# Performance work log

Hardware: AMD Instinct MI355X
Metric: run time of the kernel (lower is better)

Reference implementation:

```python
import jax, jax.numpy as jnp
import numpy as np

N, P, E = 100000, 10000, 500000
DN, DP, DK, SKIP, MLP_H = 256, 128, 100, 27, 64
E_MEAN, E_STD = 4.0, 2.0
ETA_MEAN, ETA_STD = 0.0, 1.5
ATT_NORM = 0.1  # 1/sqrt(100)
LN_EPS, RMS_EPS = 1e-5, 1e-6


def setup_inputs() -> dict:
    key = jax.random.key(0)
    ks = jax.random.split(key, 32)
    DIN = DN + SKIP  # 283
    s = 0.05
    inp = {
        'node_hidden': jax.random.normal(ks[0], (N, DN), jnp.float32),
        'energy': jax.random.uniform(ks[1], (N,), jnp.float32, 0.01, 1.0),
        'eta': jax.random.normal(ks[2], (N,), jnp.float32),
        'phi': jax.random.normal(ks[3], (N,), jnp.float32),
        'layer': jax.random.uniform(ks[4], (N,), jnp.float32),
        'eta_l': jax.random.normal(ks[5], (N, 6), jnp.float32),
        'phi_l': jax.random.normal(ks[6], (N, 6), jnp.float32),
        'ene_l': jax.random.normal(ks[7], (N, 6), jnp.float32),
        'track_feats': jax.random.uniform(ks[8], (N, 5), jnp.float32),
        'particle_hidden': jax.random.normal(ks[9], (P, DP), jnp.float32),
        'global_rep': jax.random.normal(ks[10], (P, DN), jnp.float32),
        'edge_src': jax.random.randint(ks[11], (E,), 0, N, jnp.int32),
        'edge_dst': jax.random.randint(ks[12], (E,), 0, P, jnp.int32),
        # learned params
        'W_key': jax.random.normal(ks[13], (DIN, DK), jnp.float32) * s,
        'b_key': jnp.zeros((DK,), jnp.float32),
        'W_val': jax.random.normal(ks[14], (DIN, DP), jnp.float32) * s,
        'b_val': jnp.zeros((DP,), jnp.float32),
        'W_q': jax.random.normal(ks[15], (DP + DN, DK), jnp.float32) * s,
        'b_q': jnp.zeros((DK,), jnp.float32),
        'W_ih': jax.random.normal(ks[16], (DP, 3 * DP), jnp.float32) * s,
        'b_ih': jnp.zeros((3 * DP,), jnp.float32),
        'W_hh': jax.random.normal(ks[17], (DP, 3 * DP), jnp.float32) * s,
        'b_hh': jnp.zeros((3 * DP,), jnp.float32),
        'ln_g': jnp.ones((DP,), jnp.float32),
        'ln_b': jnp.zeros((DP,), jnp.float32),
        'W1': jax.random.normal(ks[18], (DP, MLP_H), jnp.float32) * s,
        'b1': jnp.zeros((MLP_H,), jnp.float32),
        'W2': jax.random.normal(ks[19], (MLP_H, DP), jnp.float32) * s,
        'b2': jnp.zeros((DP,), jnp.float32),
        'rms_w': jnp.ones((DP,), jnp.float32),
        'lin_w': jax.random.normal(ks[20], (1, DP), jnp.float32),
    }
    return inp


def _forward(node_hidden, energy, eta, phi, layer, eta_l, phi_l, ene_l, track_feats,
             particle_hidden, global_rep,
             W_key, b_key, W_val, b_val, W_q, b_q, W_ih, b_ih, W_hh, b_hh,
             ln_g, ln_b, W1, b1, W2, b2, rms_w, lin_w, edge_src, edge_dst):
    # --- build node inputs: hidden rep + 27 skip scalars (same order as torch cat) ---
    skip = jnp.concatenate([
        ((jnp.log(energy) - E_MEAN) / E_STD)[:, None],
        ((eta - ETA_MEAN) / ETA_STD)[:, None],
        phi[:, None], layer[:, None],
        (eta_l - ETA_MEAN) / ETA_STD,  # eta_l1..l6
        phi_l, ene_l,
        track_feats,  # isTrack, nTracks, tracks_pt, nTracks_4, tracks_pt_4
    ], axis=1)  # [N, 27]
    x = jnp.concatenate([node_hidden, skip], axis=1)  # [N, 283]
    keys = x @ W_key + b_key      # [N, 100]
    vals = x @ W_val + b_val      # [N, DP]
    q = jnp.concatenate([particle_hidden, global_rep], axis=1) @ W_q + b_q  # [P, 100]

    # --- per-edge attention (note: node_update consumes RAW relu attention) ---
    att = jax.nn.relu(jnp.sum(keys[edge_src] * q[edge_dst], axis=1) * ATT_NORM)  # [E]
    msg = att[:, None] * vals[edge_src]                                          # [E, DP]
    ws = jax.ops.segment_sum(msg, edge_dst, num_segments=P)                      # [P, DP]

    # --- node update: rmsnorm * sigmoid(eltwise) gating, GRU, LN, MLP residual ---
    rms = ws * jax.lax.rsqrt(jnp.mean(ws * ws, axis=-1, keepdims=True) + RMS_EPS) * rms_w
    gated = rms * jax.nn.sigmoid(ws * lin_w)

    h = particle_hidden
    gi = gated @ W_ih + b_ih
    gh = h @ W_hh + b_hh
    i_r, i_z, i_n = jnp.split(gi, 3, axis=1)
    h_r, h_z, h_n = jnp.split(gh, 3, axis=1)
    r = jax.nn.sigmoid(i_r + h_r)
    z = jax.nn.sigmoid(i_z + h_z)
    n = jnp.tanh(i_n + r * h_n)
    h_new = (1.0 - z) * n + z * h

    mu = jnp.mean(h_new, axis=-1, keepdims=True)
    var = jnp.mean((h_new - mu) ** 2, axis=-1, keepdims=True)
    ln = (h_new - mu) * jax.lax.rsqrt(var + LN_EPS) * ln_g + ln_b
    mlp = jax.nn.relu(ln @ W1 + b1) @ W2 + b2
    return h + mlp  # updated particle 'node hidden rep'


def reference(node_hidden, energy, eta, phi, layer, eta_l, phi_l, ene_l, track_feats,
              particle_hidden, global_rep, edge_src, edge_dst,
              W_key, b_key, W_val, b_val, W_q, b_q, W_ih, b_ih, W_hh, b_hh,
              ln_g, ln_b, W1, b1, W2, b2, rms_w, lin_w):
    return _forward(node_hidden, energy, eta, phi, layer, eta_l, phi_l, ene_l, track_feats,
                    particle_hidden, global_rep,
                    W_key, b_key, W_val, b_val, W_q, b_q, W_ih, b_ih, W_hh, b_hh,
                    ln_g, ln_b, W1, b1, W2, b2, rms_w, lin_w, edge_src, edge_dst)
```

## Files before the change

kernel.cpp:

```cpp
#include <hip/hip_runtime.h>
#include <hip/hip_bf16.h>
#include <math.h>

#define THREADS 256

typedef __bf16 bf16_t;
typedef __bf16 bf16x8 __attribute__((ext_vector_type(8)));
typedef float f32x4 __attribute__((ext_vector_type(4)));

__device__ __forceinline__ float sigmoidf_(float x) { return 1.f / (1.f + expf(-x)); }

__device__ __forceinline__ void gload_lds16(const void* g, void* l) {
    __builtin_amdgcn_global_load_lds((const __attribute__((address_space(1))) void*)g,
                                     (__attribute__((address_space(3))) void*)l, 16, 0, 0);
}

__device__ __forceinline__ bf16x8 cvt8(float4 a, float4 b) {
    bf16x8 v;
    v[0] = (bf16_t)a.x; v[1] = (bf16_t)a.y; v[2] = (bf16_t)a.z; v[3] = (bf16_t)a.w;
    v[4] = (bf16_t)b.x; v[5] = (bf16_t)b.y; v[6] = (bf16_t)b.z; v[7] = (bf16_t)b.w;
    return v;
}

__global__ void prep_kernel(const float* __restrict__ W_key, const float* __restrict__ W_val,
                            const float* __restrict__ W_q, const float* __restrict__ b_key,
                            const float* __restrict__ b_val, const float* __restrict__ b_q,
                            bf16_t* __restrict__ WbfT, bf16_t* __restrict__ WqT,
                            float* __restrict__ bpn, float* __restrict__ bpq)
{
    int i = blockIdx.x * THREADS + threadIdx.x;
    const int NW = 256 * 288, NQ = 128 * 384;
    if (i < NW) {
        int c = i / 288, k = i - c * 288;
        float v = 0.f;
        if (k < 283) {
            if (c < 100) v = W_key[k * 100 + c];
            else if (c >= 128 && c < 256) v = W_val[k * 128 + (c - 128)];
        }
        WbfT[i] = (bf16_t)v;
    } else if (i < NW + NQ) {
        int j = i - NW;
        int c = j / 384, k = j - c * 384;
        WqT[j] = (bf16_t)((c < 100) ? W_q[k * 100 + c] : 0.f);
    } else if (i < NW + NQ + 256) {
        int c = i - NW - NQ;
        bpn[c] = (c < 100) ? b_key[c] : ((c >= 128 && c < 256) ? b_val[c - 128] : 0.f);
    } else if (i < NW + NQ + 256 + 128) {
        int c = i - NW - NQ - 256;
        bpq[c] = (c < 100) ? b_q[c] : 0.f;
    }
}

__global__ void prep2_kernel(const float* __restrict__ W_ih, const float* __restrict__ W_hh,
                             const float* __restrict__ b_ih, const float* __restrict__ b_hh,
                             const float* __restrict__ W1, const float* __restrict__ b1,
                             const float* __restrict__ W2,
                             bf16_t* __restrict__ BTg, bf16_t* __restrict__ W1Tp,
                             bf16_t* __restrict__ W2Tp, float* __restrict__ bgru,
                             float* __restrict__ b1p)
{
    int i = blockIdx.x * THREADS + threadIdx.x;
    const int NG = 768 * 256, N1 = 128 * 128, N2 = 128 * 128;
    if (i < NG) {
        int c = i >> 8, k = i & 255;
        float v = 0.f;
        if (c < 384) { if (k < 128) v = W_ih[k * 384 + c]; }
        else         { if (k >= 128) v = W_hh[(k - 128) * 384 + (c - 384)]; }
        BTg[i] = (bf16_t)v;
    } else if (i < NG + N1) {
        int j = i - NG; int c = j >> 7, k = j & 127;
        W1Tp[j] = (bf16_t)((c < 64) ? W1[k * 64 + c] : 0.f);
    } else if (i < NG + N1 + N2) {
        int j = i - NG - N1; int c = j >> 7, k = j & 127;
        W2Tp[j] = (bf16_t)((k < 64) ? W2[k * 128 + c] : 0.f);
    } else if (i < NG + N1 + N2 + 768) {
        int c = i - NG - N1 - N2;
        bgru[c] = (c < 384) ? b_ih[c] : b_hh[c - 384];
    } else if (i < NG + N1 + N2 + 768 + 128) {
        int c = i - NG - N1 - N2 - 768;
        b1p[c] = (c < 64) ? b1[c] : 0.f;
    }
}

__global__ void skip_kernel(const float* __restrict__ energy, const float* __restrict__ eta,
                            const float* __restrict__ phi, const float* __restrict__ layer,
                            const float* __restrict__ eta_l, const float* __restrict__ phi_l,
                            const float* __restrict__ ene_l, const float* __restrict__ track,
                            bf16_t* __restrict__ skipb, int N_, int Mpad)
{
    int n = blockIdx.x * THREADS + threadIdx.x;
    if (n >= Mpad) return;
    float o[32];
#pragma unroll
    for (int j = 0; j < 32; ++j) o[j] = 0.f;
    if (n < N_) {
        o[0] = (logf(energy[n]) - 4.0f) * 0.5f;
        o[1] = eta[n] * (1.f / 1.5f);
        o[2] = phi[n];
        o[3] = layer[n];
#pragma unroll
        for (int j = 0; j < 6; ++j) o[4 + j]  = eta_l[n * 6 + j] * (1.f / 1.5f);
#pragma unroll
        for (int j = 0; j < 6; ++j) o[10 + j] = phi_l[n * 6 + j];
#pragma unroll
        for (int j = 0; j < 6; ++j) o[16 + j] = ene_l[n * 6 + j];
#pragma unroll
        for (int j = 0; j < 5; ++j) o[22 + j] = track[n * 5 + j];
    }
    bf16_t* dst = skipb + (size_t)n * 32;
#pragma unroll
    for (int g = 0; g < 4; ++g) {
        bf16x8 v;
#pragma unroll
        for (int j = 0; j < 8; ++j) v[j] = (bf16_t)o[g * 8 + j];
        *(bf16x8*)(dst + g * 8) = v;
    }
}

template <int MODE>
__global__ __launch_bounds__(256) void mfma_gemm(
    const void* __restrict__ A0, const void* __restrict__ A1,
    const bf16_t* __restrict__ BT, const float* __restrict__ bias,
    void* __restrict__ out0v, const float* __restrict__ resid,
    int K, int Mlimit, int Nrows)
{
    __shared__ short AsS[128 * 32];
    __shared__ short BsS[128 * 32];
    int tid = threadIdx.x;
    int lane = tid & 63, w = tid >> 6;
    int la = lane & 15, hi = lane >> 4;
    int m0 = (w & 1) * 64, n0 = (w >> 1) * 64;
    int row0 = blockIdx.y * 128, col0 = blockIdx.x * 128;

    f32x4 zero4 = {0.f, 0.f, 0.f, 0.f};
    f32x4 acc[4][4];
#pragma unroll
    for (int i = 0; i < 4; ++i)
#pragma unroll
        for (int j = 0; j < 4; ++j) acc[i][j] = zero4;

    for (int kt = 0; kt < K; kt += 32) {
#pragma unroll
        for (int it = 0; it < 2; ++it) {
            int c = tid + it * 256;
            int r = c >> 2, kc = c & 3;
            int gm = row0 + r, gk = kt + kc * 8;
            if (MODE == 0) {
                if (gk < 256) {
                    bf16x8 v = {};
                    if (gm < Nrows) {
                        const float* src = (const float*)A0 + (size_t)gm * 256 + gk;
                        v = cvt8(*(const float4*)src, *(const float4*)(src + 4));
                    }
                    *(bf16x8*)((short*)AsS + (size_t)c * 8) = v;
                } else {
                    gload_lds16((const bf16_t*)A1 + (size_t)gm * 32 + (gk - 256), AsS + c * 8);
                }
            } else if (MODE == 1) {
                bf16x8 v = {};
                if (gm < Nrows) {
                    const float* src = (gk < 128)
                        ? ((const float*)A0 + (size_t)gm * 128 + gk)
                        : ((const float*)A1 + (size_t)gm * 256 + (gk - 128));
                    v = cvt8(*(const float4*)src, *(const float4*)(src + 4));
                }
                *(bf16x8*)((short*)AsS + (size_t)c * 8) = v;
            } else {
                gload_lds16((const bf16_t*)A0 + (size_t)gm * K + gk, AsS + c * 8);
            }
            gload_lds16(BT + (size_t)(col0 + r) * K + kt + kc * 8, BsS + c * 8);
        }
        __syncthreads();
        bf16x8 a[4], b[4];
#pragma unroll
        for (int i = 0; i < 4; ++i)
            a[i] = *(const bf16x8*)(AsS + (m0 + i * 16 + la) * 32 + hi * 8);
#pragma unroll
        for (int j = 0; j < 4; ++j)
            b[j] = *(const bf16x8*)(BsS + (n0 + j * 16 + la) * 32 + hi * 8);
#pragma unroll
        for (int i = 0; i < 4; ++i)
#pragma unroll
            for (int j = 0; j < 4; ++j)
                acc[i][j] = __builtin_amdgcn_mfma_f32_16x16x32_bf16(a[i], b[j], acc[i][j], 0, 0, 0);
        __syncthreads();
    }

#pragma unroll
    for (int i = 0; i < 4; ++i) {
#pragma unroll
        for (int j = 0; j < 4; ++j) {
            int col = col0 + n0 + j * 16 + la;
            float bb = bias[col];
#pragma unroll
            for (int r = 0; r < 4; ++r) {
                int row = row0 + m0 + i * 16 + hi * 4 + r;
                float v = acc[i][j][r] + bb;
                if (MODE == 0) {
                    ((bf16_t*)out0v)[(size_t)row * 256 + col] = (bf16_t)v;
                } else if (MODE == 1) {
                    ((bf16_t*)out0v)[(size_t)row * 128 + col] = (bf16_t)v;
                } else if (MODE == 2) {
                    ((float*)out0v)[(size_t)row * 768 + col] = v;
                } else if (MODE == 3) {
                    ((bf16_t*)out0v)[(size_t)row * 128 + col] = (bf16_t)fmaxf(v, 0.f);
                } else {
                    if (row < Mlimit)
                        ((float*)out0v)[(size_t)row * 128 + col] = v + resid[(size_t)row * 128 + col];
                }
            }
        }
    }
}

__global__ void zero_ints(int* __restrict__ p, int n)
{
    int i = blockIdx.x * THREADS + threadIdx.x;
    if (i < n) p[i] = 0;
}

__global__ void hist_kernel(const int* __restrict__ dst, int* __restrict__ cnt, int E_)
{
    int i = blockIdx.x * THREADS + threadIdx.x;
    if (i < E_) atomicAdd(&cnt[dst[i]], 1);
}

__global__ void scan_kernel(const int* __restrict__ cnt, int* __restrict__ offb, int P_)
{
    __shared__ int wsum[16];
    int tid = threadIdx.x;
    int lane = tid & 63, w = tid >> 6;
    int base = tid * 10;
    int c[10];
    int s = 0;
#pragma unroll
    for (int j = 0; j < 10; ++j) {
        int i = base + j;
        c[j] = (i < P_) ? cnt[i] : 0;
        s += c[j];
    }
    int pre = s;
    for (int o = 1; o < 64; o <<= 1) {
        int t = __shfl_up(pre, o);
        if (lane >= o) pre += t;
    }
    if (lane == 63) wsum[w] = pre;
    __syncthreads();
    if (w == 0 && lane < 16) {
        int v = wsum[lane];
        for (int o = 1; o < 16; o <<= 1) {
            int t = __shfl_up(v, o, 16);
            if (lane >= o) v += t;
        }
        wsum[lane] = v;
    }
    __syncthreads();
    int waveoff = (w == 0) ? 0 : wsum[w - 1];
    int run = waveoff + pre - s;
#pragma unroll
    for (int j = 0; j < 10; ++j) {
        int i = base + j;
        if (i <= P_) offb[i] = run;
        run += c[j];
    }
}

__global__ void fill_src_kernel(const int* __restrict__ dst, const int* __restrict__ src,
                                const int* __restrict__ offb, int* __restrict__ cur,
                                int* __restrict__ csrc, int E_)
{
    int i = blockIdx.x * THREADS + threadIdx.x;
    if (i < E_) {
        int d = dst[i];
        int pos = atomicAdd(&cur[d], 1);
        csrc[offb[d] + pos] = src[i];
    }
}

__global__ __launch_bounds__(256) void edge_kernel(
    const int* __restrict__ offb, const int* __restrict__ csrc,
    const bf16_t* __restrict__ KVb, const bf16_t* __restrict__ Qb,
    float* __restrict__ ws_seg, int P_)
{
    int tid = threadIdx.x;
    int p = blockIdx.x * 4 + (tid >> 6);
    if (p >= P_) return;
    int lane = tid & 63;
    int c = lane & 15, g = lane >> 4;

    bf16x8 q8 = *(const bf16x8*)(Qb + (size_t)p * 128 + c * 8);
    float qf[8];
#pragma unroll
    for (int j = 0; j < 8; ++j) qf[j] = (float)q8[j];

    int s0 = offb[p], e0 = offb[p + 1];
    float acc[8] = {};

    int i = s0 + g;
    for (; i + 12 < e0; i += 16) {
        int n0 = csrc[i], n1 = csrc[i + 4], n2 = csrc[i + 8], n3 = csrc[i + 12];
        const bf16_t* b0 = KVb + (size_t)n0 * 256 + c * 8;
        const bf16_t* b1 = KVb + (size_t)n1 * 256 + c * 8;
        const bf16_t* b2 = KVb + (size_t)n2 * 256 + c * 8;
        const bf16_t* b3 = KVb + (size_t)n3 * 256 + c * 8;
        bf16x8 k0 = *(const bf16x8*)b0, v0 = *(const bf16x8*)(b0 + 128);
        bf16x8 k1 = *(const bf16x8*)b1, v1 = *(const bf16x8*)(b1 + 128);
        bf16x8 k2 = *(const bf16x8*)b2, v2 = *(const bf16x8*)(b2 + 128);
        bf16x8 k3 = *(const bf16x8*)b3, v3 = *(const bf16x8*)(b3 + 128);
        float d0 = 0.f, d1 = 0.f, d2 = 0.f, d3 = 0.f;
#pragma unroll
        for (int j = 0; j < 8; ++j) {
            d0 += qf[j] * (float)k0[j]; d1 += qf[j] * (float)k1[j];
            d2 += qf[j] * (float)k2[j]; d3 += qf[j] * (float)k3[j];
        }
        d0 += __shfl_xor(d0, 1); d1 += __shfl_xor(d1, 1); d2 += __shfl_xor(d2, 1); d3 += __shfl_xor(d3, 1);
        d0 += __shfl_xor(d0, 2); d1 += __shfl_xor(d1, 2); d2 += __shfl_xor(d2, 2); d3 += __shfl_xor(d3, 2);
        d0 += __shfl_xor(d0, 4); d1 += __shfl_xor(d1, 4); d2 += __shfl_xor(d2, 4); d3 += __shfl_xor(d3, 4);
        d0 += __shfl_xor(d0, 8); d1 += __shfl_xor(d1, 8); d2 += __shfl_xor(d2, 8); d3 += __shfl_xor(d3, 8);
        float a0 = fmaxf(d0 * 0.1f, 0.f), a1 = fmaxf(d1 * 0.1f, 0.f);
        float a2 = fmaxf(d2 * 0.1f, 0.f), a3 = fmaxf(d3 * 0.1f, 0.f);
#pragma unroll
        for (int j = 0; j < 8; ++j)
            acc[j] += a0 * (float)v0[j] + a1 * (float)v1[j]
                    + a2 * (float)v2[j] + a3 * (float)v3[j];
    }
    for (; i < e0; i += 4) {
        int nA = csrc[i];
        const bf16_t* bA = KVb + (size_t)nA * 256 + c * 8;
        bf16x8 kA = *(const bf16x8*)bA;
        bf16x8 vA = *(const bf16x8*)(bA + 128);
        float dA = 0.f;
#pragma unroll
        for (int j = 0; j < 8; ++j) dA += qf[j] * (float)kA[j];
        dA += __shfl_xor(dA, 1);
        dA += __shfl_xor(dA, 2);
        dA += __shfl_xor(dA, 4);
        dA += __shfl_xor(dA, 8);
        float aA = fmaxf(dA * 0.1f, 0.f);
#pragma unroll
        for (int j = 0; j < 8; ++j) acc[j] += aA * (float)vA[j];
    }

#pragma unroll
    for (int j = 0; j < 8; ++j) {
        acc[j] += __shfl_xor(acc[j], 16);
        acc[j] += __shfl_xor(acc[j], 32);
    }
    if (g == 0) {
        float* op = ws_seg + (size_t)p * 128 + c * 8;
        *(float4*)op       = make_float4(acc[0], acc[1], acc[2], acc[3]);
        *(float4*)(op + 4) = make_float4(acc[4], acc[5], acc[6], acc[7]);
    }
}

__global__ void gate_kernel(const float* __restrict__ ws_seg, const float* __restrict__ ph,
                            const float* __restrict__ rms_w, const float* __restrict__ lin_w,
                            bf16_t* __restrict__ AG, int P_, int Mq)
{
    int tid = threadIdx.x;
    int g = tid >> 4, s = tid & 15;
    int p = blockIdx.x * 16 + g;
    if (p >= Mq) return;
    int cb = s * 8;
    if (p >= P_) {
        bf16x8 z = {};
        *(bf16x8*)(AG + (size_t)p * 256 + cb) = z;
        *(bf16x8*)(AG + (size_t)p * 256 + 128 + cb) = z;
        return;
    }
    const float* wp = ws_seg + (size_t)p * 128 + cb;
    float4 a = *(const float4*)wp, b = *(const float4*)(wp + 4);
    float wsv[8] = {a.x, a.y, a.z, a.w, b.x, b.y, b.z, b.w};
    float ss = 0.f;
#pragma unroll
    for (int j = 0; j < 8; ++j) ss += wsv[j] * wsv[j];
    ss += __shfl_xor(ss, 1); ss += __shfl_xor(ss, 2); ss += __shfl_xor(ss, 4); ss += __shfl_xor(ss, 8);
    float scale = rsqrtf(ss * (1.f / 128.f) + 1e-6f);
    const float* hp = ph + (size_t)p * 128 + cb;
    float4 ha = *(const float4*)hp, hb = *(const float4*)(hp + 4);
    float hv[8] = {ha.x, ha.y, ha.z, ha.w, hb.x, hb.y, hb.z, hb.w};
    bf16x8 gv, hvb;
#pragma unroll
    for (int j = 0; j < 8; ++j) {
        int c = cb + j;
        float rv = wsv[j] * scale * rms_w[c];
        gv[j] = (bf16_t)(rv * sigmoidf_(wsv[j] * lin_w[c]));
        hvb[j] = (bf16_t)hv[j];
    }
    *(bf16x8*)(AG + (size_t)p * 256 + cb) = gv;
    *(bf16x8*)(AG + (size_t)p * 256 + 128 + cb) = hvb;
}

__global__ void gru_ln_kernel(const float* __restrict__ G768, const float* __restrict__ ph,
                              const float* __restrict__ ln_g, const float* __restrict__ ln_b,
                              bf16_t* __restrict__ LNb, int P_, int Mq)
{
    int tid = threadIdx.x;
    int g = tid >> 4, s = tid & 15;
    int p = blockIdx.x * 16 + g;
    if (p >= Mq) return;
    int cb = s * 8;
    if (p >= P_) {
        bf16x8 z = {};
        *(bf16x8*)(LNb + (size_t)p * 128 + cb) = z;
        return;
    }
    const float* G = G768 + (size_t)p * 768;
    float ir[8], iz[8], in_[8], hr[8], hz[8], hn_[8], hv[8];
#pragma unroll
    for (int q = 0; q < 2; ++q) {
        float4 v;
        v = *(const float4*)(G + cb + q * 4);        ir[q*4]=v.x; ir[q*4+1]=v.y; ir[q*4+2]=v.z; ir[q*4+3]=v.w;
        v = *(const float4*)(G + 128 + cb + q * 4);  iz[q*4]=v.x; iz[q*4+1]=v.y; iz[q*4+2]=v.z; iz[q*4+3]=v.w;
        v = *(const float4*)(G + 256 + cb + q * 4);  in_[q*4]=v.x; in_[q*4+1]=v.y; in_[q*4+2]=v.z; in_[q*4+3]=v.w;
        v = *(const float4*)(G + 384 + cb + q * 4);  hr[q*4]=v.x; hr[q*4+1]=v.y; hr[q*4+2]=v.z; hr[q*4+3]=v.w;
        v = *(const float4*)(G + 512 + cb + q * 4);  hz[q*4]=v.x; hz[q*4+1]=v.y; hz[q*4+2]=v.z; hz[q*4+3]=v.w;
        v = *(const float4*)(G + 640 + cb + q * 4);  hn_[q*4]=v.x; hn_[q*4+1]=v.y; hn_[q*4+2]=v.z; hn_[q*4+3]=v.w;
        v = *(const float4*)(ph + (size_t)p * 128 + cb + q * 4);
        hv[q*4]=v.x; hv[q*4+1]=v.y; hv[q*4+2]=v.z; hv[q*4+3]=v.w;
    }
    float hn[8];
    float sm = 0.f, sq = 0.f;
#pragma unroll
    for (int j = 0; j < 8; ++j) {
        float r = sigmoidf_(ir[j] + hr[j]);
        float z = sigmoidf_(iz[j] + hz[j]);
        float n = tanhf(in_[j] + r * hn_[j]);
        hn[j] = (1.f - z) * n + z * hv[j];
        sm += hn[j]; sq += hn[j] * hn[j];
    }
    sm += __shfl_xor(sm, 1); sm += __shfl_xor(sm, 2); sm += __shfl_xor(sm, 4); sm += __shfl_xor(sm, 8);
    sq += __shfl_xor(sq, 1); sq += __shfl_xor(sq, 2); sq += __shfl_xor(sq, 4); sq += __shfl_xor(sq, 8);
    float mu = sm * (1.f / 128.f);
    float var = sq * (1.f / 128.f) - mu * mu;
    float iv = rsqrtf(var + 1e-5f);
    bf16x8 o;
#pragma unroll
    for (int j = 0; j < 8; ++j) {
        int c = cb + j;
        o[j] = (bf16_t)((hn[j] - mu) * iv * ln_g[c] + ln_b[c]);
    }
    *(bf16x8*)(LNb + (size_t)p * 128 + cb) = o;
}

extern "C" void kernel_launch(void* const* d_in, const int* in_sizes, int n_in,
                              void* d_out, int out_size, void* d_ws, size_t ws_size,
                              hipStream_t stream)
{
    const float* nh      = (const float*)d_in[0];
    const float* energy  = (const float*)d_in[1];
    const float* eta     = (const float*)d_in[2];
    const float* phi     = (const float*)d_in[3];
    const float* layer   = (const float*)d_in[4];
    const float* eta_l   = (const float*)d_in[5];
    const float* phi_l   = (const float*)d_in[6];
    const float* ene_l   = (const float*)d_in[7];
    const float* track   = (const float*)d_in[8];
    const float* ph      = (const float*)d_in[9];
    const float* grep    = (const float*)d_in[10];
    const int*   esrc    = (const int*)d_in[11];
    const int*   edst    = (const int*)d_in[12];
    const float* W_key   = (const float*)d_in[13];
    const float* b_key   = (const float*)d_in[14];
    const float* W_val   = (const float*)d_in[15];
    const float* b_val   = (const float*)d_in[16];
    const float* W_q     = (const float*)d_in[17];
    const float* b_q     = (const float*)d_in[18];
    const float* W_ih    = (const float*)d_in[19];
    const float* b_ih    = (const float*)d_in[20];
    const float* W_hh    = (const float*)d_in[21];
    const float* b_hh    = (const float*)d_in[22];
    const float* ln_g    = (const float*)d_in[23];
    const float* ln_b    = (const float*)d_in[24];
    const float* W1      = (const float*)d_in[25];
    const float* b1      = (const float*)d_in[26];
    const float* W2      = (const float*)d_in[27];
    const float* b2      = (const float*)d_in[28];
    const float* rms_w   = (const float*)d_in[29];
    const float* lin_w   = (const float*)d_in[30];

    const int N = in_sizes[1];
    const int P = in_sizes[9] / 128;
    const int E = in_sizes[11];
    const int Mpad = ((N + 127) / 128) * 128;
    const int Mq   = ((P + 127) / 128) * 128;

    char* base = (char*)d_ws;
    size_t off = 0;
    auto alloc = [&](size_t bytes) { void* p = base + off; off = (off + bytes + 255) & ~(size_t)255; return p; };
    bf16_t* skipb = (bf16_t*)alloc((size_t)Mpad * 32 * 2);
    bf16_t* WbfT  = (bf16_t*)alloc(256 * 288 * 2);
    bf16_t* WqT   = (bf16_t*)alloc(128 * 384 * 2);
    float*  bpn   = (float*)alloc(256 * 4);
    float*  bpq   = (float*)alloc(128 * 4);
    bf16_t* KVb   = (bf16_t*)alloc((size_t)Mpad * 256 * 2);
    bf16_t* Qb    = (bf16_t*)alloc((size_t)Mq * 128 * 2);
    float*  ws_seg= (float*)alloc((size_t)P * 128 * 4);
    int*    cnt   = (int*)alloc((size_t)(2 * P) * 4);
    int*    cur   = cnt + P;
    int*    offb  = (int*)alloc((size_t)(P + 1) * 4);
    int*    csrc  = (int*)alloc((size_t)E * 4);
    bf16_t* AG    = (bf16_t*)alloc((size_t)Mq * 256 * 2);
    bf16_t* BTg   = (bf16_t*)alloc(768 * 256 * 2);
    bf16_t* W1Tp  = (bf16_t*)alloc(128 * 128 * 2);
    bf16_t* W2Tp  = (bf16_t*)alloc(128 * 128 * 2);
    float*  bgru  = (float*)alloc(768 * 4);
    float*  b1p   = (float*)alloc(128 * 4);
    float*  G768  = (float*)alloc((size_t)Mq * 768 * 4);
    bf16_t* LNb   = (bf16_t*)alloc((size_t)Mq * 128 * 2);
    bf16_t* M1    = (bf16_t*)alloc((size_t)Mq * 128 * 2);

    {
        int total = 256 * 288 + 128 * 384 + 256 + 128;
        prep_kernel<<<(total + THREADS - 1) / THREADS, THREADS, 0, stream>>>(
            W_key, W_val, W_q, b_key, b_val, b_q, WbfT, WqT, bpn, bpq);
        int total2 = 768 * 256 + 128 * 128 + 128 * 128 + 768 + 128;
        prep2_kernel<<<(total2 + THREADS - 1) / THREADS, THREADS, 0, stream>>>(
            W_ih, W_hh, b_ih, b_hh, W1, b1, W2, BTg, W1Tp, W2Tp, bgru, b1p);
        skip_kernel<<<(Mpad + THREADS - 1) / THREADS, THREADS, 0, stream>>>(
            energy, eta, phi, layer, eta_l, phi_l, ene_l, track, skipb, N, Mpad);
    }
    mfma_gemm<0><<<dim3(2, Mpad / 128), THREADS, 0, stream>>>(
        nh, skipb, WbfT, bpn, KVb, nullptr, 288, 0, N);
    mfma_gemm<1><<<dim3(1, Mq / 128), THREADS, 0, stream>>>(
        ph, grep, WqT, bpq, Qb, nullptr, 384, 0, P);
    zero_ints<<<(2 * P + THREADS - 1) / THREADS, THREADS, 0, stream>>>(cnt, 2 * P);
    hist_kernel<<<(E + THREADS - 1) / THREADS, THREADS, 0, stream>>>(edst, cnt, E);
    scan_kernel<<<1, 1024, 0, stream>>>(cnt, offb, P);
    fill_src_kernel<<<(E + THREADS - 1) / THREADS, THREADS, 0, stream>>>(
        edst, esrc, offb, cur, csrc, E);
    edge_kernel<<<(P + 3) / 4, THREADS, 0, stream>>>(offb, csrc, KVb, Qb, ws_seg, P);
    gate_kernel<<<Mq / 16, THREADS, 0, stream>>>(ws_seg, ph, rms_w, lin_w, AG, P, Mq);
    mfma_gemm<2><<<dim3(6, Mq / 128), THREADS, 0, stream>>>(
        AG, nullptr, BTg, bgru, G768, nullptr, 256, 0, Mq);
    gru_ln_kernel<<<Mq / 16, THREADS, 0, stream>>>(G768, ph, ln_g, ln_b, LNb, P, Mq);
    mfma_gemm<3><<<dim3(1, Mq / 128), THREADS, 0, stream>>>(
        LNb, nullptr, W1Tp, b1p, M1, nullptr, 128, 0, Mq);
    mfma_gemm<4><<<dim3(1, Mq / 128), THREADS, 0, stream>>>(
        M1, nullptr, W2Tp, b2, d_out, ph, 128, P, Mq);
}
```

Before: 261.7 us.

## Double-buffer LDS tiles in MFMA GEMM to overlap loads with compute

Converts the GEMM's shared-memory A/B tiles into two ping-pong buffers. The next K-tile is fetched, into registers for fp32 sources or through global_load_lds for bf16, while MFMAs run on the current tile, and the barrier count drops to one per iteration. This is meant to hide global-load latency behind the matrix math. The cost is twice the LDS footprint and more live registers for the prefetched float4s, which can lower occupancy.

```diff
diff --git a/kernel.cpp b/kernel.cpp
--- a/kernel.cpp
+++ b/kernel.cpp
@@ -124,66 +124,98 @@
     void* __restrict__ out0v, const float* __restrict__ resid,
     int K, int Mlimit, int Nrows)
 {
-    __shared__ short AsS[128 * 32];
-    __shared__ short BsS[128 * 32];
+    __shared__ short AsS[2][128 * 32];
+    __shared__ short BsS[2][128 * 32];
     int tid = threadIdx.x;
     int lane = tid & 63, w = tid >> 6;
     int la = lane & 15, hi = lane >> 4;
     int m0 = (w & 1) * 64, n0 = (w >> 1) * 64;
     int row0 = blockIdx.y * 128, col0 = blockIdx.x * 128;
 
+    const int c0 = tid, c1 = tid + 256;
+    const int r0_ = c0 >> 2, k0_ = (c0 & 3) * 8;
+    const int r1_ = c1 >> 2, k1_ = (c1 & 3) * 8;
+
     f32x4 zero4 = {0.f, 0.f, 0.f, 0.f};
+    float4 zf4 = make_float4(0.f, 0.f, 0.f, 0.f);
     f32x4 acc[4][4];
 #pragma unroll
     for (int i = 0; i < 4; ++i)
 #pragma unroll
         for (int j = 0; j < 4; ++j) acc[i][j] = zero4;
 
-    for (int kt = 0; kt < K; kt += 32) {
-#pragma unroll
-        for (int it = 0; it < 2; ++it) {
-            int c = tid + it * 256;
-            int r = c >> 2, kc = c & 3;
-            int gm = row0 + r, gk = kt + kc * 8;
-            if (MODE == 0) {
-                if (gk < 256) {
-                    bf16x8 v = {};
-                    if (gm < Nrows) {
-                        const float* src = (const float*)A0 + (size_t)gm * 256 + gk;
-                        v = cvt8(*(const float4*)src, *(const float4*)(src + 4));
-                    }
-                    *(bf16x8*)((short*)AsS + (size_t)c * 8) = v;
-                } else {
-                    gload_lds16((const bf16_t*)A1 + (size_t)gm * 32 + (gk - 256), AsS + c * 8);
-                }
-            } else if (MODE == 1) {
-                bf16x8 v = {};
-                if (gm < Nrows) {
-                    const float* src = (gk < 128)
-                        ? ((const float*)A0 + (size_t)gm * 128 + gk)
-                        : ((const float*)A1 + (size_t)gm * 256 + (gk - 128));
-                    v = cvt8(*(const float4*)src, *(const float4*)(src + 4));
-                }
-                *(bf16x8*)((short*)AsS + (size_t)c * 8) = v;
-            } else {
-                gload_lds16((const bf16_t*)A0 + (size_t)gm * K + gk, AsS + c * 8);
-            }
-            gload_lds16(BT + (size_t)(col0 + r) * K + kt + kc * 8, BsS + c * 8);
+    float4 va0, va1, va2, va3;
+
+    auto issueA = [&](int kt) {
+        int gm0 = row0 + r0_, gk0 = kt + k0_;
+        int gm1 = row0 + r1_, gk1 = kt + k1_;
+        const float* s0;
+        const float* s1;
+        if (MODE == 0) {
+            s0 = (const float*)A0 + (size_t)gm0 * 256 + gk0;
+            s1 = (const float*)A0 + (size_t)gm1 * 256 + gk1;
+        } else {
+            s0 = (gk0 < 128) ? ((const float*)A0 + (size_t)gm0 * 128 + gk0)
+                             : ((const float*)A1 + (size_t)gm0 * 256 + (gk0 - 128));
+            s1 = (gk1 < 128) ? ((const float*)A0 + (size_t)gm1 * 128 + gk1)
+                             : ((const float*)A1 + (size_t)gm1 * 256 + (gk1 - 128));
         }
-        __syncthreads();
+        bool ok0 = gm0 < Nrows, ok1 = gm1 < Nrows;
+        va0 = ok0 ? *(const float4*)s0 : zf4;
+        va1 = ok0 ? *(const float4*)(s0 + 4) : zf4;
+        va2 = ok1 ? *(const float4*)s1 : zf4;
+        va3 = ok1 ? *(const float4*)(s1 + 4) : zf4;
+    };
+    auto writeA = [&](int buf) {
+        *(bf16x8*)(&AsS[buf][(size_t)c0 * 8]) = cvt8(va0, va1);
+        *(bf16x8*)(&AsS[buf][(size_t)c1 * 8]) = cvt8(va2, va3);
+    };
+    auto stageA_glds = [&](int buf, int kt) {
+        if (MODE == 0) {
+            gload_lds16((const bf16_t*)A1 + (size_t)(row0 + r0_) * 32 + (kt - 256) + k0_,
+                        &AsS[buf][(size_t)c0 * 8]);
+            gload_lds16((const bf16_t*)A1 + (size_t)(row0 + r1_) * 32 + (kt - 256) + k1_,
+                        &AsS[buf][(size_t)c1 * 8]);
+        } else {
+            gload_lds16((const bf16_t*)A0 + (size_t)(row0 + r0_) * K + kt + k0_,
+                        &AsS[buf][(size_t)c0 * 8]);
+            gload_lds16((const bf16_t*)A0 + (size_t)(row0 + r1_) * K + kt + k1_,
+                        &AsS[buf][(size_t)c1 * 8]);
+        }
+    };
+    auto stageB = [&](int buf, int kt) {
+        gload_lds16(BT + (size_t)(col0 + r0_) * K + kt + k0_, &BsS[buf][(size_t)c0 * 8]);
+        gload_lds16(BT + (size_t)(col0 + r1_) * K + kt + k1_, &BsS[buf][(size_t)c1 * 8]);
+    };
+
+    const int nt = K / 32;
+    if (MODE <= 1) { issueA(0); writeA(0); }
+    else stageA_glds(0, 0);
+    stageB(0, 0);
+    __syncthreads();
+    int cur = 0;
+    for (int t = 0; t < nt; ++t) {
+        int ktn = (t + 1) * 32;
+        bool have = (t + 1) < nt;
+        bool nreg = have && (MODE == 1 || (MODE == 0 && ktn < 256));
+        if (nreg) issueA(ktn);
+        else if (have) stageA_glds(cur ^ 1, ktn);
+        if (have) stageB(cur ^ 1, ktn);
         bf16x8 a[4], b[4];
 #pragma unroll
         for (int i = 0; i < 4; ++i)
-            a[i] = *(const bf16x8*)(AsS + (m0 + i * 16 + la) * 32 + hi * 8);
+            a[i] = *(const bf16x8*)(&AsS[cur][(m0 + i * 16 + la) * 32 + hi * 8]);
 #pragma unroll
         for (int j = 0; j < 4; ++j)
-            b[j] = *(const bf16x8*)(BsS + (n0 + j * 16 + la) * 32 + hi * 8);
+            b[j] = *(const bf16x8*)(&BsS[cur][(n0 + j * 16 + la) * 32 + hi * 8]);
 #pragma unroll
         for (int i = 0; i < 4; ++i)
 #pragma unroll
             for (int j = 0; j < 4; ++j)
                 acc[i][j] = __builtin_amdgcn_mfma_f32_16x16x32_bf16(a[i], b[j], acc[i][j], 0, 0, 0);
+        if (nreg) writeA(cur ^ 1);
         __syncthreads();
+        cur ^= 1;
     }
 
 #pragma unroll
```

Result: slower. 329.4 us (+25.9%).

## Fuse gate into edge kernel, fold zeroing into prep, halve GEMM M-tile

Applied to the files above, without the earlier changes.

The RMSNorm/sigmoid gating that gate_kernel did is now computed inside edge_kernel, which writes the bf16 AG rows directly. This removes the ws_seg fp32 round trip and one launch. Zeroing of the counters and of AG's padding rows moves into prep2_kernel, which drops the zero_ints launch. The MFMA GEMM row tile shrinks from 128 to 64, doubling the block count so the small-M GEMMs fill more CUs, at the cost of less B reuse per block.

```diff
diff --git a/kernel.cpp b/kernel.cpp
--- a/kernel.cpp
+++ b/kernel.cpp
@@ -57,10 +57,13 @@
                              const float* __restrict__ W2,
                              bf16_t* __restrict__ BTg, bf16_t* __restrict__ W1Tp,
                              bf16_t* __restrict__ W2Tp, float* __restrict__ bgru,
-                             float* __restrict__ b1p)
+                             float* __restrict__ b1p,
+                             int* __restrict__ cnt, int twoP,
+                             bf16_t* __restrict__ AG, int padStart, int padElems)
 {
     int i = blockIdx.x * THREADS + threadIdx.x;
     const int NG = 768 * 256, N1 = 128 * 128, N2 = 128 * 128;
+    const int NB = NG + N1 + N2 + 768 + 128;
     if (i < NG) {
         int c = i >> 8, k = i & 255;
         float v = 0.f;
@@ -76,9 +79,14 @@
     } else if (i < NG + N1 + N2 + 768) {
         int c = i - NG - N1 - N2;
         bgru[c] = (c < 384) ? b_ih[c] : b_hh[c - 384];
-    } else if (i < NG + N1 + N2 + 768 + 128) {
+    } else if (i < NB) {
         int c = i - NG - N1 - N2 - 768;
         b1p[c] = (c < 64) ? b1[c] : 0.f;
+    } else if (i < NB + twoP) {
+        cnt[i - NB] = 0;
+    } else if (i < NB + twoP + padElems) {
+        int j = i - NB - twoP;
+        AG[(size_t)padStart * 256 + j] = (bf16_t)0.f;
     }
 }
 
@@ -124,62 +132,65 @@
     void* __restrict__ out0v, const float* __restrict__ resid,
     int K, int Mlimit, int Nrows)
 {
-    __shared__ short AsS[128 * 32];
+    __shared__ short AsS[64 * 32];
     __shared__ short BsS[128 * 32];
     int tid = threadIdx.x;
     int lane = tid & 63, w = tid >> 6;
     int la = lane & 15, hi = lane >> 4;
-    int m0 = (w & 1) * 64, n0 = (w >> 1) * 64;
-    int row0 = blockIdx.y * 128, col0 = blockIdx.x * 128;
+    int m0 = (w & 1) * 32, n0 = (w >> 1) * 64;
+    int row0 = blockIdx.y * 64, col0 = blockIdx.x * 128;
 
     f32x4 zero4 = {0.f, 0.f, 0.f, 0.f};
-    f32x4 acc[4][4];
-#pragma unroll
-    for (int i = 0; i < 4; ++i)
+    f32x4 acc[2][4];
+#pragma unroll
+    for (int i = 0; i < 2; ++i)
 #pragma unroll
         for (int j = 0; j < 4; ++j) acc[i][j] = zero4;
 
+    const int ra = tid >> 2, ka = (tid & 3) * 8;
+    const int c1 = tid + 256;
+    const int rb0 = tid >> 2, kb0 = (tid & 3) * 8;
+    const int rb1 = c1 >> 2,  kb1 = (c1 & 3) * 8;
+
     for (int kt = 0; kt < K; kt += 32) {
-#pragma unroll
-        for (int it = 0; it < 2; ++it) {
-            int c = tid + it * 256;
-            int r = c >> 2, kc = c & 3;
-            int gm = row0 + r, gk = kt + kc * 8;
-            if (MODE == 0) {
-                if (gk < 256) {
-                    bf16x8 v = {};
-                    if (gm < Nrows) {
-                        const float* src = (const float*)A0 + (size_t)gm * 256 + gk;
-                        v = cvt8(*(const float4*)src, *(const float4*)(src + 4));
-                    }
-                    *(bf16x8*)((short*)AsS + (size_t)c * 8) = v;
-                } else {
-                    gload_lds16((const bf16_t*)A1 + (size_t)gm * 32 + (gk - 256), AsS + c * 8);
+        int gmA = row0 + ra;
+        if (MODE == 0) {
+            if (kt < 256) {
+                bf16x8 v = {};
+                if (gmA < Nrows) {
+                    const float* s = (const float*)A0 + (size_t)gmA * 256 + kt + ka;
+                    v = cvt8(*(const float4*)s, *(const float4*)(s + 4));
                 }
-            } else if (MODE == 1) {
-                bf16x8 v = {};
-                if (gm < Nrows) {
-                    const float* src = (gk < 128)
-                        ? ((const float*)A0 + (size_t)gm * 128 + gk)
-                        : ((const float*)A1 + (size_t)gm * 256 + (gk - 128));
-                    v = cvt8(*(const float4*)src, *(const float4*)(src + 4));
-                }
-                *(bf16x8*)((short*)AsS + (size_t)c * 8) = v;
+                *(bf16x8*)(AsS + (size_t)tid * 8) = v;
             } else {
-                gload_lds16((const bf16_t*)A0 + (size_t)gm * K + gk, AsS + c * 8);
+                gload_lds16((const bf16_t*)A1 + (size_t)gmA * 32 + (kt - 256) + ka,
+                            AsS + (size_t)tid * 8);
             }
-            gload_lds16(BT + (size_t)(col0 + r) * K + kt + kc * 8, BsS + c * 8);
+        } else if (MODE == 1) {
+            int gk = kt + ka;
+            bf16x8 v = {};
+            if (gmA < Nrows) {
+                const float* s = (gk < 128) ? ((const float*)A0 + (size_t)gmA * 128 + gk)
+                                            : ((const float*)A1 + (size_t)gmA * 256 + (gk - 128));
+                v = cvt8(*(const float4*)s, *(const float4*)(s + 4));
+            }
+            *(bf16x8*)(AsS + (size_t)tid * 8) = v;
+        } else {
+            gload_lds16((const bf16_t*)A0 + (size_t)gmA * K + kt + ka,
+                        AsS + (size_t)tid * 8);
         }
+        gload_lds16(BT + (size_t)(col0 + rb0) * K + kt + kb0, BsS + (size_t)tid * 8);
+        gload_lds16(BT + (size_t)(col0 + rb1) * K + kt + kb1, BsS + (size_t)c1 * 8);
         __syncthreads();
-        bf16x8 a[4], b[4];
-#pragma unroll
-        for (int i = 0; i < 4; ++i)
+        bf16x8 a[2], b[4];
+#pragma unroll
+        for (int i = 0; i < 2; ++i)
             a[i] = *(const bf16x8*)(AsS + (m0 + i * 16 + la) * 32 + hi * 8);
 #pragma unroll
         for (int j = 0; j < 4; ++j)
             b[j] = *(const bf16x8*)(BsS + (n0 + j * 16 + la) * 32 + hi * 8);
 #pragma unroll
-        for (int i = 0; i < 4; ++i)
+        for (int i = 0; i < 2; ++i)
 #pragma unroll
             for (int j = 0; j < 4; ++j)
                 acc[i][j] = __builtin_amdgcn_mfma_f32_16x16x32_bf16(a[i], b[j], acc[i][j], 0, 0, 0);
@@ -187,7 +198,7 @@
     }
 
 #pragma unroll
-    for (int i = 0; i < 4; ++i) {
+    for (int i = 0; i < 2; ++i) {
 #pragma unroll
         for (int j = 0; j < 4; ++j) {
             int col = col0 + n0 + j * 16 + la;
@@ -213,12 +224,6 @@
     }
 }
 
-__global__ void zero_ints(int* __restrict__ p, int n)
-{
-    int i = blockIdx.x * THREADS + threadIdx.x;
-    if (i < n) p[i] = 0;
-}
-
 __global__ void hist_kernel(const int* __restrict__ dst, int* __restrict__ cnt, int E_)
 {
     int i = blockIdx.x * THREADS + threadIdx.x;
@@ -280,7 +285,8 @@
 __global__ __launch_bounds__(256) void edge_kernel(
     const int* __restrict__ offb, const int* __restrict__ csrc,
     const bf16_t* __restrict__ KVb, const bf16_t* __restrict__ Qb,
-    float* __restrict__ ws_seg, int P_)
+    const float* __restrict__ ph, const float* __restrict__ rms_w,
+    const float* __restrict__ lin_w, bf16_t* __restrict__ AG, int P_)
 {
     int tid = threadIdx.x;
     int p = blockIdx.x * 4 + (tid >> 6);
@@ -346,49 +352,28 @@
         acc[j] += __shfl_xor(acc[j], 16);
         acc[j] += __shfl_xor(acc[j], 32);
     }
-    if (g == 0) {
-        float* op = ws_seg + (size_t)p * 128 + c * 8;
-        *(float4*)op       = make_float4(acc[0], acc[1], acc[2], acc[3]);
-        *(float4*)(op + 4) = make_float4(acc[4], acc[5], acc[6], acc[7]);
-    }
-}
-
-__global__ void gate_kernel(const float* __restrict__ ws_seg, const float* __restrict__ ph,
-                            const float* __restrict__ rms_w, const float* __restrict__ lin_w,
-                            bf16_t* __restrict__ AG, int P_, int Mq)
-{
-    int tid = threadIdx.x;
-    int g = tid >> 4, s = tid & 15;
-    int p = blockIdx.x * 16 + g;
-    if (p >= Mq) return;
-    int cb = s * 8;
-    if (p >= P_) {
-        bf16x8 z = {};
-        *(bf16x8*)(AG + (size_t)p * 256 + cb) = z;
-        *(bf16x8*)(AG + (size_t)p * 256 + 128 + cb) = z;
-        return;
-    }
-    const float* wp = ws_seg + (size_t)p * 128 + cb;
-    float4 a = *(const float4*)wp, b = *(const float4*)(wp + 4);
-    float wsv[8] = {a.x, a.y, a.z, a.w, b.x, b.y, b.z, b.w};
+
     float ss = 0.f;
 #pragma unroll
-    for (int j = 0; j < 8; ++j) ss += wsv[j] * wsv[j];
+    for (int j = 0; j < 8; ++j) ss += acc[j] * acc[j];
     ss += __shfl_xor(ss, 1); ss += __shfl_xor(ss, 2); ss += __shfl_xor(ss, 4); ss += __shfl_xor(ss, 8);
     float scale = rsqrtf(ss * (1.f / 128.f) + 1e-6f);
-    const float* hp = ph + (size_t)p * 128 + cb;
-    float4 ha = *(const float4*)hp, hb = *(const float4*)(hp + 4);
-    float hv[8] = {ha.x, ha.y, ha.z, ha.w, hb.x, hb.y, hb.z, hb.w};
-    bf16x8 gv, hvb;
-#pragma unroll
-    for (int j = 0; j < 8; ++j) {
-        int c = cb + j;
-        float rv = wsv[j] * scale * rms_w[c];
-        gv[j] = (bf16_t)(rv * sigmoidf_(wsv[j] * lin_w[c]));
-        hvb[j] = (bf16_t)hv[j];
-    }
-    *(bf16x8*)(AG + (size_t)p * 256 + cb) = gv;
-    *(bf16x8*)(AG + (size_t)p * 256 + 128 + cb) = hvb;
+    if (g == 0) {
+        int cb = c * 8;
+        const float* hp = ph + (size_t)p * 128 + cb;
+        float4 ha = *(const float4*)hp, hb = *(const float4*)(hp + 4);
+        float hv[8] = {ha.x, ha.y, ha.z, ha.w, hb.x, hb.y, hb.z, hb.w};
+        bf16x8 gv, hvb;
+#pragma unroll
+        for (int j = 0; j < 8; ++j) {
+            float wsv = acc[j];
+            float rv = wsv * scale * rms_w[cb + j];
+            gv[j] = (bf16_t)(rv * sigmoidf_(wsv * lin_w[cb + j]));
+            hvb[j] = (bf16_t)hv[j];
+        }
+        *(bf16x8*)(AG + (size_t)p * 256 + cb) = gv;
+        *(bf16x8*)(AG + (size_t)p * 256 + 128 + cb) = hvb;
+    }
 }
 
 __global__ void gru_ln_kernel(const float* __restrict__ G768, const float* __restrict__ ph,
@@ -495,7 +480,6 @@
     float*  bpq   = (float*)alloc(128 * 4);
     bf16_t* KVb   = (bf16_t*)alloc((size_t)Mpad * 256 * 2);
     bf16_t* Qb    = (bf16_t*)alloc((size_t)Mq * 128 * 2);
-    float*  ws_seg= (float*)alloc((size_t)P * 128 * 4);
     int*    cnt   = (int*)alloc((size_t)(2 * P) * 4);
     int*    cur   = cnt + P;
     int*    offb  = (int*)alloc((size_t)(P + 1) * 4);
@@ -514,28 +498,29 @@
         int total = 256 * 288 + 128 * 384 + 256 + 128;
         prep_kernel<<<(total + THREADS - 1) / THREADS, THREADS, 0, stream>>>(
             W_key, W_val, W_q, b_key, b_val, b_q, WbfT, WqT, bpn, bpq);
-        int total2 = 768 * 256 + 128 * 128 + 128 * 128 + 768 + 128;
+        int padElems = (Mq - P) * 256;
+        int total2 = 768 * 256 + 128 * 128 + 128 * 128 + 768 + 128 + 2 * P + padElems;
         prep2_kernel<<<(total2 + THREADS - 1) / THREADS, THREADS, 0, stream>>>(
-            W_ih, W_hh, b_ih, b_hh, W1, b1, W2, BTg, W1Tp, W2Tp, bgru, b1p);
+            W_ih, W_hh, b_ih, b_hh, W1, b1, W2, BTg, W1Tp, W2Tp, bgru, b1p,
+            cnt, 2 * P, AG, P, padElems);
         skip_kernel<<<(Mpad + THREADS - 1) / THREADS, THREADS, 0, stream>>>(
             energy, eta, phi, layer, eta_l, phi_l, ene_l, track, skipb, N, Mpad);
     }
-    mfma_gemm<0><<<dim3(2, Mpad / 128), THREADS, 0, stream>>>(
+    mfma_gemm<0><<<dim3(2, Mpad / 64), THREADS, 0, stream>>>(
         nh, skipb, WbfT, bpn, KVb, nullptr, 288, 0, N);
-    mfma_gemm<1><<<dim3(1, Mq / 128), THREADS, 0, stream>>>(
+    mfma_gemm<1><<<dim3(1, Mq / 64), THREADS, 0, stream>>>(
         ph, grep, WqT, bpq, Qb, nullptr, 384, 0, P);
-    zero_ints<<<(2 * P + THREADS - 1) / THREADS, THREADS, 0, stream>>>(cnt, 2 * P);
     hist_kernel<<<(E + THREADS - 1) / THREADS, THREADS, 0, stream>>>(edst, cnt, E);
     scan_kernel<<<1, 1024, 0, stream>>>(cnt, offb, P);
     fill_src_kernel<<<(E + THREADS - 1) / THREADS, THREADS, 0, stream>>>(
         edst, esrc, offb, cur, csrc, E);
-    edge_kernel<<<(P + 3) / 4, THREADS, 0, stream>>>(offb, csrc, KVb, Qb, ws_seg, P);
-    gate_kernel<<<Mq / 16, THREADS, 0, stream>>>(ws_seg, ph, rms_w, lin_w, AG, P, Mq);
-    mfma_gemm<2><<<dim3(6, Mq / 128), THREADS, 0, stream>>>(
+    edge_kernel<<<(P + 3) / 4, THREADS, 0, stream>>>(
+        offb, csrc, KVb, Qb, ph, rms_w, lin_w, AG, P);
+    mfma_gemm<2><<<dim3(6, Mq / 64), THREADS, 0, stream>>>(
         AG, nullptr, BTg, bgru, G768, nullptr, 256, 0, Mq);
     gru_ln_kernel<<<Mq / 16, THREADS, 0, stream>>>(G768, ph, ln_g, ln_b, LNb, P, Mq);
-    mfma_gemm<3><<<dim3(1, Mq / 128), THREADS, 0, stream>>>(
+    mfma_gemm<3><<<dim3(1, Mq / 64), THREADS, 0, stream>>>(
         LNb, nullptr, W1Tp, b1p, M1, nullptr, 128, 0, Mq);
-    mfma_gemm<4><<<dim3(1, Mq / 128), THREADS, 0, stream>>>(
+    mfma_gemm<4><<<dim3(1, Mq / 64), THREADS, 0, stream>>>(
         M1, nullptr, W2Tp, b2, d_out, ph, 128, P, Mq);
 }
```

Result: faster. 231.1 us (-11.7%).
